# Performance work log

Measured on AMD Instinct MI355X. Metric: run time of the kernel, lower is better.

The kernel has to match this reference:

```python
import jax, jax.numpy as jnp
import numpy as np

B, S, E, H, D, NE, R = 2, 2048, 2048, 16, 128, 8, 16
HALF = D // 2
THETA = 10000.0


def setup_inputs() -> dict:
    key = jax.random.key(0)
    ks = jax.random.split(key, 18)

    def w(k, shape, fan_in):
        return jax.random.normal(k, shape, jnp.float32) / np.float32(np.sqrt(fan_in))

    inp = {
        "x": jax.random.normal(ks[0], (B, S, E), jnp.float32),
        "expert_mask": jax.random.uniform(ks[1], (B, S, NE), dtype=jnp.float32),
    }
    for i, n in enumerate(("q", "k", "v")):
        inp["W" + n] = w(ks[2 + 3 * i], (H * D, E), E)
        inp["b" + n] = jnp.zeros((H * D,), jnp.float32)
        inp["A" + n] = w(ks[3 + 3 * i], (NE, R, E), E)
        inp["B" + n] = w(ks[4 + 3 * i], (H * D, NE, R), R)
    inp["Wo"] = w(ks[11], (E, H * D), H * D)
    inp["bo"] = jnp.zeros((E,), jnp.float32)
    inp["Ao"] = w(ks[12], (NE, R, H * D), H * D)
    inp["Bo"] = w(ks[13], (E, NE, R), R)
    return inp


def routed_linear(x, W, b, A, Bm, mask):
    """MaybeRoutedLinear: dense base + expert-routed low-rank path gated by mask [B,S,NE]."""
    y = jnp.einsum("bsi,oi->bso", x, W) + b
    h = jnp.einsum("bsi,eri->bser", x, A) * mask[..., None]  # [B,S,NE,R]
    return y + jnp.einsum("bser,oer->bso", h, Bm)


def apply_rope(t):
    """Llama-style rotary embedding. t: [B,S,H,D]."""
    inv_freq = 1.0 / (THETA ** (jnp.arange(0, D, 2, dtype=jnp.float32) / D))  # [D/2]
    freqs = jnp.arange(S, dtype=jnp.float32)[:, None] * inv_freq[None, :]  # [S,D/2]
    cos = jnp.concatenate([jnp.cos(freqs)] * 2, -1)[None, :, None, :]  # [1,S,1,D]
    sin = jnp.concatenate([jnp.sin(freqs)] * 2, -1)[None, :, None, :]
    rot = jnp.concatenate([-t[..., HALF:], t[..., :HALF]], -1)
    return t * cos + rot * sin


def reference(x, expert_mask, Wq, bq, Aq, Bq, Wk, bk, Ak, Bk, Wv, bv, Av, Bv, Wo, bo, Ao, Bo):
    q = routed_linear(x, Wq, bq, Aq, Bq, expert_mask).reshape(B, S, H, D)
    k = routed_linear(x, Wk, bk, Ak, Bk, expert_mask).reshape(B, S, H, D)
    v = routed_linear(x, Wv, bv, Av, Bv, expert_mask).reshape(B, S, H, D)
    q = apply_rope(q)
    k = apply_rope(k)
    scores = jnp.einsum("bqhd,bkhd->bhqk", q, k) / jnp.float32(np.sqrt(D))
    causal = jnp.tril(jnp.ones((S, S), dtype=bool))
    scores = jnp.where(causal[None, None], scores, jnp.finfo(scores.dtype).min)
    probs = jax.nn.softmax(scores, axis=-1)
    o = jnp.einsum("bhqk,bkhd->bqhd", probs, v).reshape(B, S, H * D)
    return routed_linear(o, Wo, bo, Ao, Bo, expert_mask)
```

## Files before the change

kernel.cpp:

```cpp
#include <hip/hip_runtime.h>


#define B_ 2
#define S_ 2048
#define E_ 2048
#define H_ 16
#define D_ 128
#define NE_ 8
#define R_ 16
#define HD_ 2048
#define M_ 4096
#define KL_ 128

typedef unsigned short u16;
typedef unsigned int u32;
typedef __attribute__((ext_vector_type(8))) short bf16x8;
typedef __attribute__((ext_vector_type(4))) float f32x4;

typedef const __attribute__((address_space(1))) void gvoid_t;
typedef __attribute__((address_space(3))) void svoid_t;

__device__ __forceinline__ float bf2f(u16 u) {
    union { u32 i; float f; } v; v.i = ((u32)u) << 16; return v.f;
}
__device__ __forceinline__ u16 f2bf(float f) {
    union { float f; u32 i; } v; v.f = f;
    u32 x = v.i;
    return (u16)((x + 0x7fffu + ((x >> 16) & 1u)) >> 16);
}
__device__ __forceinline__ float ldf(const void* p, size_t i, int f) {
    return f ? ((const float*)p)[i] : bf2f(((const u16*)p)[i]);
}
__device__ __forceinline__ float4 ld4(const void* p, size_t i, int f) {
    if (f) return *(const float4*)((const float*)p + i);
    ushort4 v = *(const ushort4*)((const u16*)p + i);
    return make_float4(bf2f(v.x), bf2f(v.y), bf2f(v.z), bf2f(v.w));
}

__global__ void k_detect(const void* __restrict__ x, int* __restrict__ flags) {
    __shared__ int votes[2];
    int tid = threadIdx.x;
    if (tid < 2) votes[tid] = 0;
    __syncthreads();
    const u32* p = (const u32*)x;
    int bad = 0, tot = 0;
    for (int i = tid; i < 4096; i += 64) {
        u32 lo = p[i] & 0xffffu;
        if (lo) {
            tot++;
            int e = (int)((lo >> 7) & 0xffu);
            if (e < 100 || e > 150) bad++;
        }
    }
    atomicAdd(&votes[0], bad);
    atomicAdd(&votes[1], tot);
    __syncthreads();
    if (tid == 0) flags[0] = (votes[1] > 0 && votes[0] * 10 > votes[1] * 3) ? 1 : 0;
}

__global__ void k_cvt(const void* __restrict__ src, u16* __restrict__ dst, int n,
                      const int* __restrict__ flags) {
    int fin = flags[0];
    int i = (blockIdx.x * 256 + threadIdx.x) * 4;
    if (i >= n) return;
    float4 v = ld4(src, i, fin);
    ushort4 o;
    o.x = f2bf(v.x); o.y = f2bf(v.y); o.z = f2bf(v.z); o.w = f2bf(v.w);
    *(ushort4*)(dst + i) = o;
}

__global__ void k_cvtf(const float* __restrict__ src, u16* __restrict__ dst, int n) {
    int i = (blockIdx.x * 256 + threadIdx.x) * 4;
    if (i >= n) return;
    float4 v = *(const float4*)(src + i);
    ushort4 o;
    o.x = f2bf(v.x); o.y = f2bf(v.y); o.z = f2bf(v.z); o.w = f2bf(v.w);
    *(ushort4*)(dst + i) = o;
}

__global__ void k_zero(float4* __restrict__ p, int n4) {
    int i = blockIdx.x * 256 + threadIdx.x;
    if (i < n4) p[i] = make_float4(0.f, 0.f, 0.f, 0.f);
}

#define NX_  8388608L
#define NA1_ 262144L
#define NW_  4194304L
__global__ void k_cvt_all(
    const void* __restrict__ x,
    const void* __restrict__ Aq, const void* __restrict__ Ak,
    const void* __restrict__ Av, const void* __restrict__ Ao,
    const void* __restrict__ Bq, const void* __restrict__ Bk,
    const void* __restrict__ Bv, const void* __restrict__ Bo,
    const void* __restrict__ Wq, const void* __restrict__ Wk,
    const void* __restrict__ Wv,
    u16* __restrict__ Xb, u16* __restrict__ Acat, u16* __restrict__ Bmcat,
    u16* __restrict__ Wcat,
    const int* __restrict__ flags) {
    int fin = flags[0];
    long i = (long)(blockIdx.x * 256 + threadIdx.x) * 4;
    const void* src; u16* dst; long off;
    if (i < NX_) { src = x; dst = Xb; off = i; }
    else if (i < NX_ + 4 * NA1_) {
        long j = i - NX_; int p = (int)(j >> 18); off = j & (NA1_ - 1);
        src = (p == 0) ? Aq : (p == 1) ? Ak : (p == 2) ? Av : Ao;
        dst = Acat + (long)p * NA1_;
    } else if (i < NX_ + 8 * NA1_) {
        long j = i - NX_ - 4 * NA1_; int p = (int)(j >> 18); off = j & (NA1_ - 1);
        src = (p == 0) ? Bq : (p == 1) ? Bk : (p == 2) ? Bv : Bo;
        dst = Bmcat + (long)p * NA1_;
    } else {
        long j = i - NX_ - 8 * NA1_; int p = (int)(j / NW_); off = j - (long)p * NW_;
        src = (p == 0) ? Wq : (p == 1) ? Wk : Wv;
        dst = Wcat + (long)p * NW_;
    }
    float4 v = ld4(src, off, fin);
    ushort4 o;
    o.x = f2bf(v.x); o.y = f2bf(v.y); o.z = f2bf(v.z); o.w = f2bf(v.w);
    *(ushort4*)(dst + off) = o;
}

#define BM_ 128
#define BN_ 128
#define BK_ 64

__global__ __launch_bounds__(256, 2) void k_gemm_sk(
    const u16* __restrict__ A, int lda,
    const u16* __restrict__ Bw, int ldb, int K,
    const void* __restrict__ mask,
    float* __restrict__ Cf, int ldc,
    const int* __restrict__ flags) {
    __shared__ __align__(16) u16 As[BM_ * BK_];
    __shared__ __align__(16) u16 Bs[BN_ * BK_];
    int fin = flags[0];
    int tid = threadIdx.x;
    int w = tid >> 6, lane = tid & 63;
    int l15 = lane & 15, quad = lane >> 4;
    int wm = w >> 1, wn = w & 1;
    int m0 = blockIdx.y * BM_, n0 = blockIdx.x * BN_;
    int lrow = lane >> 3;
    int lcol = (lane & 7) * 8;

    f32x4 acc[4][4];
#pragma unroll
    for (int mt = 0; mt < 4; mt++)
#pragma unroll
        for (int nt = 0; nt < 4; nt++)
#pragma unroll
            for (int r = 0; r < 4; r++) acc[mt][nt][r] = 0.f;

    int iters = (K / BK_) / gridDim.z;
    int it0 = blockIdx.z * iters;
    for (int it = it0; it < it0 + iters; it++) {
        int kb = it * BK_;
        __syncthreads();
#pragma unroll
        for (int i = 0; i < 4; i++) {
            int rowb = (w * 4 + i) * 8;
            int r = rowb + lrow;
            __builtin_amdgcn_global_load_lds(
                (gvoid_t*)(A + (size_t)(m0 + r) * lda + kb + lcol),
                (svoid_t*)(As + rowb * BK_), 16, 0, 0);
            __builtin_amdgcn_global_load_lds(
                (gvoid_t*)(Bw + (size_t)(n0 + r) * ldb + kb + lcol),
                (svoid_t*)(Bs + rowb * BK_), 16, 0, 0);
        }
        __syncthreads();
#pragma unroll
        for (int kk = 0; kk < 2; kk++) {
            int ko = kk * 32 + quad * 8;
            bf16x8 af[4], bf[4];
#pragma unroll
            for (int mt = 0; mt < 4; mt++)
                af[mt] = *(const bf16x8*)(As + (wm * 64 + mt * 16 + l15) * BK_ + ko);
#pragma unroll
            for (int nt = 0; nt < 4; nt++)
                bf[nt] = *(const bf16x8*)(Bs + (wn * 64 + nt * 16 + l15) * BK_ + ko);
#pragma unroll
            for (int mt = 0; mt < 4; mt++)
#pragma unroll
                for (int nt = 0; nt < 4; nt++)
                    acc[mt][nt] = __builtin_amdgcn_mfma_f32_16x16x32_bf16(
                        af[mt], bf[nt], acc[mt][nt], 0, 0, 0);
        }
    }

#pragma unroll
    for (int mt = 0; mt < 4; mt++) {
#pragma unroll
        for (int r = 0; r < 4; r++) {
            int m = m0 + wm * 64 + mt * 16 + quad * 4 + r;
#pragma unroll
            for (int nt = 0; nt < 4; nt++) {
                int n = n0 + wn * 64 + nt * 16 + l15;
                float v = acc[mt][nt][r] * ldf(mask, (size_t)m * NE_ + ((n & 127) >> 4), fin);
                atomicAdd(&Cf[(size_t)m * ldc + n], v);
            }
        }
    }
}

template <int BMt>
__global__ __launch_bounds__(512, 2) void k_gemm8p(
    const u16* __restrict__ A, int lda,
    const u16* __restrict__ Bw, int ldb, int K1,
    const u16* __restrict__ A2, int lda2,
    const u16* __restrict__ B2, int K2,
    const void* __restrict__ bias0, const void* __restrict__ bias1,
    const void* __restrict__ bias2,
    void* __restrict__ C, int ldc, int store_mode,
    const int* __restrict__ flags) {
    constexpr int MT  = BMt / 32;
    constexpr int NSA = BMt / 16;
    constexpr int LA  = BMt / 128;
    constexpr int L   = LA + 2;
    __shared__ __align__(16) u16 As[4][NSA * 512];
    __shared__ __align__(16) u16 Bs[4][16 * 512];
    int fin = flags[0];
    int tid = threadIdx.x;
    int w = tid >> 6, lane = tid & 63;
    int l15 = lane & 15, quad = lane >> 4;
    int wm = w >> 2, wn = w & 3;

    int lin = blockIdx.y * gridDim.x + blockIdx.x;
    int cpx = (gridDim.x * gridDim.y) >> 3;
    int wg = (lin & 7) * cpx + (lin >> 3);
    int m0 = (wg / gridDim.x) * BMt;
    int n0 = (wg % gridDim.x) * 256;

    int p = (store_mode == 3) ? (n0 >> 11) : 0;
    const u16* A2p = A2 + p * 128;
    const u16* B2p = B2 + (long)p * NA1_;
    int nloc = (store_mode == 3) ? (n0 & 2047) : n0;

    int nk1 = K1 >> 5;
    int NT = nk1 + (K2 >> 5);

    f32x4 acc[MT][4];
#pragma unroll
    for (int mt = 0; mt < MT; mt++)
#pragma unroll
        for (int nt = 0; nt < 4; nt++)
#pragma unroll
            for (int r = 0; r < 4; r++) acc[mt][nt][r] = 0.f;

    auto stageA = [&](int kt) {
        const u16* pa; size_t sa; int kb;
        if (kt < nk1) { pa = A;   sa = (size_t)lda;  kb = kt * 32; }
        else          { pa = A2p; sa = (size_t)lda2; kb = (kt - nk1) * 32; }
        int buf = kt & 3;
#pragma unroll
        for (int j = 0; j < LA; j++) {
            int rb = w * LA + j;
            __builtin_amdgcn_global_load_lds(
                (gvoid_t*)(pa + (size_t)(m0 + rb * 16 + l15) * sa + kb + quad * 8),
                (svoid_t*)(&As[buf][rb * 512]), 16, 0, 0);
        }
    };
    auto stageB = [&](int kt) {
        const u16* pb; size_t sb; int kb, nb;
        if (kt < nk1) { pb = Bw;  sb = (size_t)ldb; kb = kt * 32;          nb = n0; }
        else          { pb = B2p; sb = (size_t)K2;  kb = (kt - nk1) * 32;  nb = nloc; }
        int buf = kt & 3;
#pragma unroll
        for (int j = 0; j < 2; j++) {
            int rb = w * 2 + j;
            __builtin_amdgcn_global_load_lds(
                (gvoid_t*)(pb + (size_t)(nb + rb * 16 + l15) * sb + kb + quad * 8),
                (svoid_t*)(&Bs[buf][rb * 512]), 16, 0, 0);
        }
    };

    stageA(0); stageB(0);
    stageA(1); stageB(1);
    stageA(2); stageB(2);
    if constexpr (L == 4) asm volatile("s_waitcnt vmcnt(8)" ::: "memory");
    else                  asm volatile("s_waitcnt vmcnt(6)" ::: "memory");
    __builtin_amdgcn_s_barrier();

    for (int kt = 0; kt < NT; kt++) {
        int buf = kt & 3;
        bool pre = (kt + 3 < NT);

        bf16x8 af[MT], bfr[4];
#pragma unroll
        for (int mt = 0; mt < MT; mt++)
            af[mt] = *(const bf16x8*)(&As[buf][(wm * MT + mt) * 512 + lane * 8]);
        bfr[0] = *(const bf16x8*)(&Bs[buf][(wn * 4 + 0) * 512 + lane * 8]);
        bfr[1] = *(const bf16x8*)(&Bs[buf][(wn * 4 + 1) * 512 + lane * 8]);
        if (pre) stageA(kt + 3);
        __builtin_amdgcn_s_barrier();
        asm volatile("s_waitcnt lgkmcnt(0)" ::: "memory");
        __builtin_amdgcn_s_setprio(1);
#pragma unroll
        for (int mt = 0; mt < MT; mt++) {
            acc[mt][0] = __builtin_amdgcn_mfma_f32_16x16x32_bf16(af[mt], bfr[0], acc[mt][0], 0, 0, 0);
            acc[mt][1] = __builtin_amdgcn_mfma_f32_16x16x32_bf16(af[mt], bfr[1], acc[mt][1], 0, 0, 0);
        }
        __builtin_amdgcn_s_setprio(0);
        __builtin_amdgcn_s_barrier();

        bfr[2] = *(const bf16x8*)(&Bs[buf][(wn * 4 + 2) * 512 + lane * 8]);
        bfr[3] = *(const bf16x8*)(&Bs[buf][(wn * 4 + 3) * 512 + lane * 8]);
        if (pre) stageB(kt + 3);
        __builtin_amdgcn_s_barrier();
        asm volatile("s_waitcnt lgkmcnt(0)" ::: "memory");
        __builtin_amdgcn_s_setprio(1);
#pragma unroll
        for (int mt = 0; mt < MT; mt++) {
            acc[mt][2] = __builtin_amdgcn_mfma_f32_16x16x32_bf16(af[mt], bfr[2], acc[mt][2], 0, 0, 0);
            acc[mt][3] = __builtin_amdgcn_mfma_f32_16x16x32_bf16(af[mt], bfr[3], acc[mt][3], 0, 0, 0);
        }
        __builtin_amdgcn_s_setprio(0);
        if (kt + 4 <= NT) {
            if constexpr (L == 4) asm volatile("s_waitcnt vmcnt(8)" ::: "memory");
            else                  asm volatile("s_waitcnt vmcnt(6)" ::: "memory");
        } else if (kt + 3 == NT) {
            if constexpr (L == 4) asm volatile("s_waitcnt vmcnt(4)" ::: "memory");
            else                  asm volatile("s_waitcnt vmcnt(3)" ::: "memory");
        } else if (kt + 2 == NT) {
            asm volatile("s_waitcnt vmcnt(0)" ::: "memory");
        }
        __builtin_amdgcn_s_barrier();
    }

    const void* bp = (store_mode == 3) ? (p == 0 ? bias0 : p == 1 ? bias1 : bias2)
                                       : bias0;
#pragma unroll
    for (int mt = 0; mt < MT; mt++) {
#pragma unroll
        for (int r = 0; r < 4; r++) {
            int m = m0 + wm * (BMt / 2) + mt * 16 + quad * 4 + r;
#pragma unroll
            for (int nt = 0; nt < 4; nt++) {
                int n = n0 + wn * 64 + nt * 16 + l15;
                float v = acc[mt][nt][r];
                if (bp) v += ldf(bp, (size_t)(n & 2047), fin);
                if (store_mode == 3) {
                    ((u16*)C)[(size_t)p * 8388608 + (size_t)m * 2048 + (n & 2047)] = f2bf(v);
                } else {
                    if (fin) ((float*)C)[(size_t)m * ldc + n] = v;
                    else     ((u16*)C)[(size_t)m * ldc + n] = f2bf(v);
                }
            }
        }
    }
}

__global__ void k_rope2(u16* __restrict__ Q, u16* __restrict__ K) {
    const int n = M_ * HD_ / 2;
    int idx = blockIdx.x * 256 + threadIdx.x;
    u16* Y = (idx < n) ? Q : K;
    int id = (idx < n) ? idx : idx - n;
    int d2 = id & 63;
    int sh = id >> 6;
    int s = (sh >> 4) & (S_ - 1);
    float inv = powf(10000.f, -(float)d2 * (1.f / 64.f));
    float fr = (float)s * inv;
    float c, sn;
    sincosf(fr, &sn, &c);
    size_t base = ((size_t)sh) << 7;
    float t0 = bf2f(Y[base + d2]);
    float t1 = bf2f(Y[base + d2 + 64]);
    Y[base + d2]      = f2bf(t0 * c - t1 * sn);
    Y[base + d2 + 64] = f2bf(t1 * c + t0 * sn);
}

__global__ void k_transpose_v(const u16* __restrict__ Vb, u16* __restrict__ Vt) {
    __shared__ u16 t[32][33];
    int s0 = blockIdx.x * 32;
    int n0 = blockIdx.y * 32;
    int b  = blockIdx.z;
    int tx = threadIdx.x & 31, ty = threadIdx.x >> 5;
#pragma unroll
    for (int r = 0; r < 4; r++)
        t[ty + r * 8][tx] = Vb[((size_t)(b * S_ + s0 + ty + r * 8)) * HD_ + n0 + tx];
    __syncthreads();
#pragma unroll
    for (int r = 0; r < 4; r++)
        Vt[((size_t)(b * HD_ + n0 + ty + r * 8)) * S_ + s0 + tx] = t[tx][ty + r * 8];
}

#define KS_ST 136
#define VT_ST 72
#define SCALE_ 0.088388347648318447f

__global__ __launch_bounds__(256, 3) void k_flash6(
    const u16* __restrict__ Q, const u16* __restrict__ K,
    const u16* __restrict__ Vt, u16* __restrict__ O) {
    __shared__ __align__(16) u16 Ks[64 * KS_ST];
    __shared__ __align__(16) u16 Vs[128 * VT_ST];
    __shared__ __align__(16) u16 Ps[64 * VT_ST];
    int tid = threadIdx.x;
    int w = tid >> 6, lane = tid & 63;
    int l15 = lane & 15, quad = lane >> 4;
    int bh = blockIdx.y, b = bh >> 4, h = bh & 15;
    int t = 31 - blockIdx.x;
    int q0 = t * 64;

    int krow[4], kd8[4], vd[4], vkg[4];
#pragma unroll
    for (int it = 0; it < 4; it++) {
        int idx = it * 256 + tid;
        krow[it] = idx >> 4; kd8[it] = (idx & 15) * 8;
        vd[it] = idx >> 3;   vkg[it] = (idx & 7) * 8;
    }

    bf16x8 qf[4];
    size_t baseQ = ((size_t)(b * S_ + q0 + w * 16 + l15)) * HD_ + h * D_;
#pragma unroll
    for (int ks = 0; ks < 4; ks++)
        qf[ks] = *(const bf16x8*)(Q + baseQ + ks * 32 + quad * 8);

    f32x4 of[8];
#pragma unroll
    for (int nt = 0; nt < 8; nt++)
#pragma unroll
        for (int r = 0; r < 4; r++) of[nt][r] = 0.f;
    float mreg = -30000.f, lreg = 0.f;
    int qrow = q0 + w * 16 + l15;

    int nch = t + 1;

    bf16x8 kpre[4], vpre[4];
#pragma unroll
    for (int it = 0; it < 4; it++) {
        kpre[it] = *(const bf16x8*)(K + ((size_t)(b * S_ + krow[it])) * HD_ + h * D_ + kd8[it]);
        vpre[it] = *(const bf16x8*)(Vt + ((size_t)(bh * 128 + vd[it])) * S_ + vkg[it]);
    }

    for (int c = 0; c < nch; c++) {
        int k0 = c * 64;
        __syncthreads();
#pragma unroll
        for (int it = 0; it < 4; it++) {
            *(bf16x8*)(Ks + krow[it] * KS_ST + kd8[it]) = kpre[it];
            *(bf16x8*)(Vs + vd[it] * VT_ST + vkg[it]) = vpre[it];
        }
        __syncthreads();
        if (c + 1 < nch) {
            int k1 = k0 + 64;
#pragma unroll
            for (int it = 0; it < 4; it++) {
                kpre[it] = *(const bf16x8*)(K + ((size_t)(b * S_ + k1 + krow[it])) * HD_ + h * D_ + kd8[it]);
                vpre[it] = *(const bf16x8*)(Vt + ((size_t)(bh * 128 + vd[it])) * S_ + k1 + vkg[it]);
            }
        }

        f32x4 sf[4];
#pragma unroll
        for (int nt = 0; nt < 4; nt++)
#pragma unroll
            for (int r = 0; r < 4; r++) sf[nt][r] = 0.f;
#pragma unroll
        for (int ks = 0; ks < 4; ks++) {
            int koff = ks * 32 + quad * 8;
            bf16x8 qa = qf[ks];
#pragma unroll
            for (int nt = 0; nt < 4; nt++) {
                bf16x8 kb = *(const bf16x8*)(Ks + (nt * 16 + l15) * KS_ST + koff);
                sf[nt] = __builtin_amdgcn_mfma_f32_16x16x32_bf16(kb, qa, sf[nt], 0, 0, 0);
            }
        }

#pragma unroll
        for (int nt = 0; nt < 4; nt++) {
            int keyb = k0 + nt * 16 + quad * 4;
#pragma unroll
            for (int r = 0; r < 4; r++) {
                float sv = sf[nt][r] * SCALE_;
                sf[nt][r] = (keyb + r > qrow) ? -30000.f : sv;
            }
        }

        float t0 = fmaxf(fmaxf(sf[0][0], sf[0][1]), fmaxf(sf[0][2], sf[0][3]));
        float t1 = fmaxf(fmaxf(sf[1][0], sf[1][1]), fmaxf(sf[1][2], sf[1][3]));
        float t2 = fmaxf(fmaxf(sf[2][0], sf[2][1]), fmaxf(sf[2][2], sf[2][3]));
        float t3 = fmaxf(fmaxf(sf[3][0], sf[3][1]), fmaxf(sf[3][2], sf[3][3]));
        float cmax = fmaxf(fmaxf(t0, t1), fmaxf(t2, t3));
        cmax = fmaxf(cmax, __shfl_xor(cmax, 16, 64));
        cmax = fmaxf(cmax, __shfl_xor(cmax, 32, 64));
        float mnew = fmaxf(mreg, cmax);
        float a = __expf(mreg - mnew);
        mreg = mnew;
#pragma unroll
        for (int nt = 0; nt < 4; nt++)
#pragma unroll
            for (int r = 0; r < 4; r++)
                sf[nt][r] = __expf(sf[nt][r] - mnew);
        float s0 = (sf[0][0] + sf[0][1]) + (sf[0][2] + sf[0][3]);
        float s1 = (sf[1][0] + sf[1][1]) + (sf[1][2] + sf[1][3]);
        float s2 = (sf[2][0] + sf[2][1]) + (sf[2][2] + sf[2][3]);
        float s3 = (sf[3][0] + sf[3][1]) + (sf[3][2] + sf[3][3]);
        float psum = (s0 + s1) + (s2 + s3);
        psum += __shfl_xor(psum, 16, 64);
        psum += __shfl_xor(psum, 32, 64);
        lreg = lreg * a + psum;

        float al[4];
#pragma unroll
        for (int r = 0; r < 4; r++) al[r] = __shfl(a, quad * 4 + r, 16);

#pragma unroll
        for (int nt = 0; nt < 4; nt++)
#pragma unroll
            for (int r = 0; r < 4; r++)
                Ps[(w * 16 + l15) * VT_ST + nt * 16 + quad * 4 + r] = f2bf(sf[nt][r]);
#pragma unroll
        for (int nt = 0; nt < 8; nt++)
#pragma unroll
            for (int r = 0; r < 4; r++) of[nt][r] *= al[r];

#pragma unroll
        for (int ks2 = 0; ks2 < 2; ks2++) {
            int koff = ks2 * 32 + quad * 8;
            bf16x8 pa = *(const bf16x8*)(Ps + (w * 16 + l15) * VT_ST + koff);
#pragma unroll
            for (int nt = 0; nt < 8; nt++) {
                bf16x8 vb = *(const bf16x8*)(Vs + (nt * 16 + l15) * VT_ST + koff);
                of[nt] = __builtin_amdgcn_mfma_f32_16x16x32_bf16(pa, vb, of[nt], 0, 0, 0);
            }
        }
    }

    float linv = 1.f / lreg;
    float inv[4];
#pragma unroll
    for (int r = 0; r < 4; r++) inv[r] = __shfl(linv, quad * 4 + r, 16);
    int rowb = q0 + w * 16 + quad * 4;
#pragma unroll
    for (int r = 0; r < 4; r++) {
        size_t base = ((size_t)(b * S_ + rowb + r)) * HD_ + h * D_;
#pragma unroll
        for (int nt = 0; nt < 8; nt++)
            O[base + nt * 16 + l15] = f2bf(of[nt][r] * inv[r]);
    }
}

extern "C" void kernel_launch(void* const* d_in, const int* in_sizes, int n_in,
                              void* d_out, int out_size, void* d_ws, size_t ws_size,
                              hipStream_t stream) {
    const void* x    = d_in[0];
    const void* mask = d_in[1];
    const void* Wq = d_in[2];  const void* bq = d_in[3];
    const void* Aq = d_in[4];  const void* Bq = d_in[5];
    const void* Wk = d_in[6];  const void* bk = d_in[7];
    const void* Ak = d_in[8];  const void* Bk = d_in[9];
    const void* Wv = d_in[10]; const void* bv = d_in[11];
    const void* Av = d_in[12]; const void* Bv = d_in[13];
    const void* Wo = d_in[14]; const void* bo = d_in[15];
    const void* Ao = d_in[16]; const void* Bo = d_in[17];

    char* ws = (char*)d_ws;
    const long MB = 1 << 20;
    int* flags = (int*)ws;
    u16* Xb    = (u16*)(ws + 1  * MB);
    u16* Acat  = (u16*)(ws + 17 * MB);
    u16* Bmcat = (u16*)(ws + 19 * MB);
    u16* hg3   = (u16*)(ws + 21 * MB);
    u16* hgo   = (u16*)(ws + 24 * MB);
    u16* Qb    = (u16*)(ws + 25 * MB);
    u16* Kb    = (u16*)(ws + 41 * MB);
    u16* Vb    = (u16*)(ws + 57 * MB);
    u16* Vt    = (u16*)(ws + 73 * MB);
    u16* Wcat  = (u16*)(ws + 73 * MB);
    float* hg3f = (float*)Qb;
    float* hgof = (float*)Kb;
    u16* Wob   = Qb;
    u16* Ob    = Vb;

    k_detect<<<1, 64, 0, stream>>>(x, flags);
    k_zero<<<1536, 256, 0, stream>>>((float4*)hg3f, 393216);
    const long NCVT = NX_ + 8 * NA1_ + 3 * NW_;
    k_cvt_all<<<NCVT / 1024, 256, 0, stream>>>(
        x, Aq, Ak, Av, Ao, Bq, Bk, Bv, Bo, Wq, Wk, Wv,
        Xb, Acat, Bmcat, Wcat, flags);

    k_gemm_sk<<<dim3(3, M_ / BM_, 4), 256, 0, stream>>>(
        Xb, E_, Acat, E_, E_, mask, hg3f, 384, flags);
    k_cvtf<<<1536, 256, 0, stream>>>(hg3f, hg3, 1572864);

    k_gemm8p<256><<<dim3(6144 / 256, M_ / 256), 512, 0, stream>>>(
        Xb, E_, Wcat, E_, E_, hg3, 384, Bmcat, KL_,
        bq, bk, bv, Qb, HD_, 3, flags);

    k_rope2<<<(M_ * HD_) / 256, 256, 0, stream>>>(Qb, Kb);
    k_transpose_v<<<dim3(S_ / 32, HD_ / 32, B_), 256, 0, stream>>>(Vb, Vt);

    k_flash6<<<dim3(32, 32), 256, 0, stream>>>(Qb, Kb, Vt, Ob);

    k_zero<<<512, 256, 0, stream>>>((float4*)hgof, 131072);
    k_cvt<<<NW_ / 1024, 256, 0, stream>>>(Wo, Wob, (int)NW_, flags);
    k_gemm_sk<<<dim3(1, M_ / BM_, 4), 256, 0, stream>>>(
        Ob, HD_, Acat + 3 * NA1_, E_, E_, mask, hgof, KL_, flags);
    k_cvtf<<<512, 256, 0, stream>>>(hgof, hgo, 524288);

    k_gemm8p<128><<<dim3(HD_ / 256, M_ / 128), 512, 0, stream>>>(
        Ob, HD_, Wob, E_, E_, hgo, KL_, Bmcat + 3 * NA1_, KL_,
        bo, nullptr, nullptr, d_out, HD_, 2, flags);
}
```

Measured before the change: 728.7 us.

## Double-buffer flash K/V prefetch, remap flash blocks, vectorize rope, add sched barriers

The flash attention kernel now prefetches K/V two chunks ahead using two register buffers, and remaps block indices so that consecutive blocks interleave heads and causal lengths. The rope kernel computes sin/cos once per (row, frequency group) and reuses it across all heads for both Q and K, using 4-wide vector loads. Sched barriers are added in the GEMM mainloop to stop the compiler from moving MFMAs across the waitcnt. The aim is to hide global latency and cut the redundant transcendental work, at the cost of extra registers in flash (occupancy risk) and far fewer rope blocks.

```diff
diff --git a/kernel.cpp b/kernel.cpp
--- a/kernel.cpp
+++ b/kernel.cpp
@@ -291,6 +291,7 @@
         if (pre) stageA(kt + 3);
         __builtin_amdgcn_s_barrier();
         asm volatile("s_waitcnt lgkmcnt(0)" ::: "memory");
+        __builtin_amdgcn_sched_barrier(0);
         __builtin_amdgcn_s_setprio(1);
 #pragma unroll
         for (int mt = 0; mt < MT; mt++) {
@@ -305,6 +306,7 @@
         if (pre) stageB(kt + 3);
         __builtin_amdgcn_s_barrier();
         asm volatile("s_waitcnt lgkmcnt(0)" ::: "memory");
+        __builtin_amdgcn_sched_barrier(0);
         __builtin_amdgcn_s_setprio(1);
 #pragma unroll
         for (int mt = 0; mt < MT; mt++) {
@@ -347,23 +349,48 @@
     }
 }
 
-__global__ void k_rope2(u16* __restrict__ Q, u16* __restrict__ K) {
-    const int n = M_ * HD_ / 2;
+__global__ void k_rope3(u16* __restrict__ Q, u16* __restrict__ K) {
     int idx = blockIdx.x * 256 + threadIdx.x;
-    u16* Y = (idx < n) ? Q : K;
-    int id = (idx < n) ? idx : idx - n;
-    int d2 = id & 63;
-    int sh = id >> 6;
-    int s = (sh >> 4) & (S_ - 1);
-    float inv = powf(10000.f, -(float)d2 * (1.f / 64.f));
-    float fr = (float)s * inv;
-    float c, sn;
-    sincosf(fr, &sn, &c);
-    size_t base = ((size_t)sh) << 7;
-    float t0 = bf2f(Y[base + d2]);
-    float t1 = bf2f(Y[base + d2 + 64]);
-    Y[base + d2]      = f2bf(t0 * c - t1 * sn);
-    Y[base + d2 + 64] = f2bf(t1 * c + t0 * sn);
+    int d2g = idx & 15;
+    int rs  = idx >> 4;
+    int s   = rs & (S_ - 1);
+    float cs[4], sn[4];
+#pragma unroll
+    for (int j = 0; j < 4; j++) {
+        int d2 = d2g * 4 + j;
+        float inv = powf(10000.f, -(float)d2 * (1.f / 64.f));
+        float fr = (float)s * inv;
+        sincosf(fr, &sn[j], &cs[j]);
+    }
+#pragma unroll
+    for (int h = 0; h < H_; h++) {
+        size_t base = ((size_t)(rs * H_ + h)) << 7;
+#pragma unroll
+        for (int a = 0; a < 2; a++) {
+            u16* Y = a ? K : Q;
+            ushort4 lo = *(const ushort4*)(Y + base + d2g * 4);
+            ushort4 hi = *(const ushort4*)(Y + base + 64 + d2g * 4);
+            ushort4 lo2, hi2;
+            {
+                float t0 = bf2f(lo.x), t1 = bf2f(hi.x);
+                lo2.x = f2bf(t0 * cs[0] - t1 * sn[0]); hi2.x = f2bf(t1 * cs[0] + t0 * sn[0]);
+            }
+            {
+                float t0 = bf2f(lo.y), t1 = bf2f(hi.y);
+                lo2.y = f2bf(t0 * cs[1] - t1 * sn[1]); hi2.y = f2bf(t1 * cs[1] + t0 * sn[1]);
+            }
+            {
+                float t0 = bf2f(lo.z), t1 = bf2f(hi.z);
+                lo2.z = f2bf(t0 * cs[2] - t1 * sn[2]); hi2.z = f2bf(t1 * cs[2] + t0 * sn[2]);
+            }
+            {
+                float t0 = bf2f(lo.w), t1 = bf2f(hi.w);
+                lo2.w = f2bf(t0 * cs[3] - t1 * sn[3]); hi2.w = f2bf(t1 * cs[3] + t0 * sn[3]);
+            }
+            *(ushort4*)(Y + base + d2g * 4) = lo2;
+            *(ushort4*)(Y + base + 64 + d2g * 4) = hi2;
+        }
+    }
 }
 
 __global__ void k_transpose_v(const u16* __restrict__ Vb, u16* __restrict__ Vt) {
@@ -385,7 +412,7 @@
 #define VT_ST 72
 #define SCALE_ 0.088388347648318447f
 
-__global__ __launch_bounds__(256, 3) void k_flash6(
+__global__ __launch_bounds__(256, 3) void k_flash7(
     const u16* __restrict__ Q, const u16* __restrict__ K,
     const u16* __restrict__ Vt, u16* __restrict__ O) {
     __shared__ __align__(16) u16 Ks[64 * KS_ST];
@@ -394,8 +421,11 @@
     int tid = threadIdx.x;
     int w = tid >> 6, lane = tid & 63;
     int l15 = lane & 15, quad = lane >> 4;
-    int bh = blockIdx.y, b = bh >> 4, h = bh & 15;
-    int t = 31 - blockIdx.x;
+
+    int lin = blockIdx.y * 32 + blockIdx.x;
+    int wg  = (lin & 7) * 128 + (lin >> 3);
+    int bh = wg >> 5, b = bh >> 4, h = bh & 15;
+    int t = 31 - (wg & 31);
     int q0 = t * 64;
 
     int krow[4], kd8[4], vd[4], vkg[4];
@@ -422,28 +452,51 @@
 
     int nch = t + 1;
 
-    bf16x8 kpre[4], vpre[4];
+    bf16x8 kpA[4], vpA[4], kpB[4], vpB[4];
 #pragma unroll
     for (int it = 0; it < 4; it++) {
-        kpre[it] = *(const bf16x8*)(K + ((size_t)(b * S_ + krow[it])) * HD_ + h * D_ + kd8[it]);
-        vpre[it] = *(const bf16x8*)(Vt + ((size_t)(bh * 128 + vd[it])) * S_ + vkg[it]);
+        kpA[it] = *(const bf16x8*)(K + ((size_t)(b * S_ + krow[it])) * HD_ + h * D_ + kd8[it]);
+        vpA[it] = *(const bf16x8*)(Vt + ((size_t)(bh * 128 + vd[it])) * S_ + vkg[it]);
+    }
+    if (nch > 1) {
+#pragma unroll
+        for (int it = 0; it < 4; it++) {
+            kpB[it] = *(const bf16x8*)(K + ((size_t)(b * S_ + 64 + krow[it])) * HD_ + h * D_ + kd8[it]);
+            vpB[it] = *(const bf16x8*)(Vt + ((size_t)(bh * 128 + vd[it])) * S_ + 64 + vkg[it]);
+        }
     }
 
     for (int c = 0; c < nch; c++) {
         int k0 = c * 64;
         __syncthreads();
-#pragma unroll
-        for (int it = 0; it < 4; it++) {
-            *(bf16x8*)(Ks + krow[it] * KS_ST + kd8[it]) = kpre[it];
-            *(bf16x8*)(Vs + vd[it] * VT_ST + vkg[it]) = vpre[it];
+        if ((c & 1) == 0) {
+#pragma unroll
+            for (int it = 0; it < 4; it++) {
+                *(bf16x8*)(Ks + krow[it] * KS_ST + kd8[it]) = kpA[it];
+                *(bf16x8*)(Vs + vd[it] * VT_ST + vkg[it]) = vpA[it];
+            }
+        } else {
+#pragma unroll
+            for (int it = 0; it < 4; it++) {
+                *(bf16x8*)(Ks + krow[it] * KS_ST + kd8[it]) = kpB[it];
+                *(bf16x8*)(Vs + vd[it] * VT_ST + vkg[it]) = vpB[it];
+            }
         }
         __syncthreads();
-        if (c + 1 < nch) {
-            int k1 = k0 + 64;
-#pragma unroll
-            for (int it = 0; it < 4; it++) {
-                kpre[it] = *(const bf16x8*)(K + ((size_t)(b * S_ + k1 + krow[it])) * HD_ + h * D_ + kd8[it]);
-                vpre[it] = *(const bf16x8*)(Vt + ((size_t)(bh * 128 + vd[it])) * S_ + k1 + vkg[it]);
+        if (c + 2 < nch) {
+            int k2 = k0 + 128;
+            if ((c & 1) == 0) {
+#pragma unroll
+                for (int it = 0; it < 4; it++) {
+                    kpA[it] = *(const bf16x8*)(K + ((size_t)(b * S_ + k2 + krow[it])) * HD_ + h * D_ + kd8[it]);
+                    vpA[it] = *(const bf16x8*)(Vt + ((size_t)(bh * 128 + vd[it])) * S_ + k2 + vkg[it]);
+                }
+            } else {
+#pragma unroll
+                for (int it = 0; it < 4; it++) {
+                    kpB[it] = *(const bf16x8*)(K + ((size_t)(b * S_ + k2 + krow[it])) * HD_ + h * D_ + kd8[it]);
+                    vpB[it] = *(const bf16x8*)(Vt + ((size_t)(bh * 128 + vd[it])) * S_ + k2 + vkg[it]);
+                }
             }
         }
 
@@ -584,10 +637,10 @@
         Xb, E_, Wcat, E_, E_, hg3, 384, Bmcat, KL_,
         bq, bk, bv, Qb, HD_, 3, flags);
 
-    k_rope2<<<(M_ * HD_) / 256, 256, 0, stream>>>(Qb, Kb);
+    k_rope3<<<256, 256, 0, stream>>>(Qb, Kb);
     k_transpose_v<<<dim3(S_ / 32, HD_ / 32, B_), 256, 0, stream>>>(Vb, Vt);
 
-    k_flash6<<<dim3(32, 32), 256, 0, stream>>>(Qb, Kb, Vt, Ob);
+    k_flash7<<<dim3(32, 32), 256, 0, stream>>>(Qb, Kb, Vt, Ob);
 
     k_zero<<<512, 256, 0, stream>>>((float4*)hgof, 131072);
     k_cvt<<<NW_ / 1024, 256, 0, stream>>>(Wo, Wob, (int)NW_, flags);
```

Measured after the change: 720.9 us. Within noise of the previous version (-1.1%).
